# Optimization experiments

Hardware: AMD Instinct MI355X
Metric: run time of the kernel (lower is better)

## Reference

```python
import jax, jax.numpy as jnp
import numpy as np

N = 100_000        # nodes
E = 1_600_000      # edges (avg degree 16)
D_IN = 128         # raw node feature dim
H = 64             # hidden dim
D_E = 8            # edge attr dim
C = 2              # classes for both heads (parity-game winner / strategy)


def setup_inputs() -> dict:
    key = jax.random.key(0)
    ks = jax.random.split(key, 16)
    rn = lambda k, shp, s: jax.random.normal(k, shp, jnp.float32) * s
    inv = lambda f: 1.0 / np.sqrt(f)
    return {
        "x": rn(ks[0], (N, D_IN), 1.0),
        "edge_index": jax.random.randint(ks[1], (2, E), 0, N),
        "edge_attr": rn(ks[2], (E, D_E), 1.0),
        # encode: Linear(D_IN -> H) + ReLU
        "W_enc": rn(ks[3], (D_IN, H), inv(D_IN)),
        "b_enc": jnp.zeros((H,), jnp.float32),
        # core: single-head GATConv
        "W_gat": rn(ks[4], (H, H), inv(H)),
        "a_src": rn(ks[5], (H,), inv(H)),
        "a_dst": rn(ks[6], (H,), inv(H)),
        # node_classifier: MLP H -> H -> C
        "Wn1": rn(ks[7], (H, H), inv(H)),
        "bn1": jnp.zeros((H,), jnp.float32),
        "Wn2": rn(ks[8], (H, C), inv(H)),
        "bn2": jnp.zeros((C,), jnp.float32),
        # edge_classifier: MLP (2H + D_E) -> H -> C
        "We1": rn(ks[9], (2 * H + D_E, H), inv(2 * H + D_E)),
        "be1": jnp.zeros((H,), jnp.float32),
        "We2": rn(ks[10], (H, C), inv(H)),
        "be2": jnp.zeros((C,), jnp.float32),
    }


def _gat_core(h, src, dst, W_gat, a_src, a_dst):
    # Single-head GAT layer with segment softmax over incoming edges per dst.
    hg = h @ W_gat                                    # [N, H]
    hs, hd = hg[src], hg[dst]                         # [E, H] gathers
    scores = jax.nn.leaky_relu(hs @ a_src + hd @ a_dst, 0.2)  # [E]
    m = jax.ops.segment_max(scores, dst, num_segments=N)      # [N]
    m = jnp.where(jnp.isneginf(m), 0.0, m)            # guard isolated nodes
    ex = jnp.exp(scores - m[dst])                     # [E]
    denom = jax.ops.segment_sum(ex, dst, num_segments=N)      # [N]
    alpha = ex / (denom[dst] + 1e-9)                  # [E]
    agg = jax.ops.segment_sum(alpha[:, None] * hs, dst, num_segments=N)  # [N, H]
    return jax.nn.relu(agg)


def reference(x, edge_index, edge_attr, W_enc, b_enc, W_gat, a_src, a_dst,
              Wn1, bn1, Wn2, bn2, We1, be1, We2, be2):
    src, dst = edge_index[0], edge_index[1]
    # encode
    h = jax.nn.relu(x @ W_enc + b_enc)                # [N, H]
    # core (GATConv)
    xc = _gat_core(h, src, dst, W_gat, a_src, a_dst)  # [N, H]
    # node head
    node_logits = jax.nn.relu(xc @ Wn1 + bn1) @ Wn2 + bn2        # [N, C]
    # gather src/dst + concat edge_attr, edge head
    edge_feat = jnp.concatenate([xc[src], xc[dst], edge_attr], axis=-1)  # [E, 2H+D_E]
    edge_logits = jax.nn.relu(edge_feat @ We1 + be1) @ We2 + be2  # [E, C]
    return node_logits, edge_logits
```

## Files before the change

### kernel.cpp

```cpp
#include <hip/hip_runtime.h>
#include <hip/hip_bf16.h>

#define NN   100000
#define EE   1600000
#define DIN  128
#define HH   64
#define DEA  8
#define NCLS 2
#define BSZ  128
#define NBUCK ((NN + BSZ - 1) / BSZ)
#define CAPG 2368
#define CAP  4096
#define NCHUNK 100
#define CHUNK (EE / NCHUNK)

typedef __hip_bfloat16 bf16;
typedef short  short8 __attribute__((ext_vector_type(8)));
typedef float  f32x4  __attribute__((ext_vector_type(4)));

__device__ __forceinline__ void bf2x(unsigned u, float& lo, float& hi) {
    union { unsigned i; float f; } a, b;
    a.i = u << 16; b.i = u & 0xffff0000u;
    lo = a.f; hi = b.f;
}
__device__ __forceinline__ short f2bs(float f) {
    unsigned u = __float_as_uint(f);
    return (short)((u + 0x7fffu + ((u >> 16) & 1u)) >> 16);
}
__device__ __forceinline__ short8 cvt8(float4 a, float4 b) {
    short8 r;
    r[0] = f2bs(a.x); r[1] = f2bs(a.y); r[2] = f2bs(a.z); r[3] = f2bs(a.w);
    r[4] = f2bs(b.x); r[5] = f2bs(b.y); r[6] = f2bs(b.z); r[7] = f2bs(b.w);
    return r;
}
__device__ __forceinline__ f32x4 z4() {
    f32x4 z; z[0] = 0.f; z[1] = 0.f; z[2] = 0.f; z[3] = 0.f; return z;
}

#define WE_STRIDE 136
#define WG_STRIDE 72
#define TB_STRIDE 68
__global__ __launch_bounds__(256) void k_encode(
        const float* __restrict__ x,
        const float* __restrict__ W_enc, const float* __restrict__ b_enc,
        const float* __restrict__ W_gat,
        const float* __restrict__ a_src, const float* __restrict__ a_dst,
        bf16* __restrict__ hg_, float* __restrict__ s_src, float* __restrict__ s_dst) {
    __shared__ short wencT[64 * WE_STRIDE];
    __shared__ short wgatT[64 * WG_STRIDE];
    __shared__ float tb[4][16 * TB_STRIDE];
    short* hg = (short*)hg_;
    int tid = threadIdx.x;
    for (int i = tid; i < DIN * HH; i += 256) {
        int k = i >> 6, n = i & 63;
        wencT[n * WE_STRIDE + k] = f2bs(W_enc[i]);
    }
    for (int i = tid; i < HH * HH; i += 256) {
        int k = i >> 6, n = i & 63;
        wgatT[n * WG_STRIDE + k] = f2bs(W_gat[i]);
    }
    __syncthreads();
    int w = tid >> 6, l = tid & 63, m = l & 15, h = l >> 4;
    short8 wg[2][4];
    #pragma unroll
    for (int kt = 0; kt < 2; kt++)
        #pragma unroll
        for (int nt = 0; nt < 4; nt++)
            wg[kt][nt] = *(short8*)&wgatT[(nt * 16 + m) * WG_STRIDE + kt * 32 + h * 8];
    float avs[4], avd[4], ben[4];
    #pragma unroll
    for (int nt = 0; nt < 4; nt++) {
        avs[nt] = a_src[nt * 16 + m];
        avd[nt] = a_dst[nt * 16 + m];
        ben[nt] = b_enc[nt * 16 + m];
    }
    int tp = blockIdx.x * 4 + w;
    if (tp >= NN / 32) return;
    int n0 = tp * 32;
    float* tbw = tb[w];

    f32x4 acc1[2][4];
    #pragma unroll
    for (int rt = 0; rt < 2; rt++)
        #pragma unroll
        for (int nt = 0; nt < 4; nt++) acc1[rt][nt] = z4();
    #pragma unroll
    for (int kt = 0; kt < 4; kt++) {
        short8 af[2];
        #pragma unroll
        for (int rt = 0; rt < 2; rt++) {
            const float* xp = &x[(size_t)(n0 + rt * 16 + m) * DIN + kt * 32 + h * 8];
            af[rt] = cvt8(*(const float4*)xp, *(const float4*)(xp + 4));
        }
        #pragma unroll
        for (int nt = 0; nt < 4; nt++) {
            short8 bf = *(short8*)&wencT[(nt * 16 + m) * WE_STRIDE + kt * 32 + h * 8];
            acc1[0][nt] = __builtin_amdgcn_mfma_f32_16x16x32_bf16(af[0], bf, acc1[0][nt], 0, 0, 0);
            acc1[1][nt] = __builtin_amdgcn_mfma_f32_16x16x32_bf16(af[1], bf, acc1[1][nt], 0, 0, 0);
        }
    }
    #pragma unroll
    for (int rt = 0; rt < 2; rt++) {
        #pragma unroll
        for (int nt = 0; nt < 4; nt++)
            #pragma unroll
            for (int r = 0; r < 4; r++) {
                float hv = fmaxf(acc1[rt][nt][r] + ben[nt], 0.f);
                tbw[(h * 4 + r) * TB_STRIDE + nt * 16 + m] = hv;
            }
        f32x4 acc2[4];
        #pragma unroll
        for (int nt = 0; nt < 4; nt++) acc2[nt] = z4();
        #pragma unroll
        for (int kt = 0; kt < 2; kt++) {
            const float* tp_ = &tbw[m * TB_STRIDE + kt * 32 + h * 8];
            short8 af2 = cvt8(*(const float4*)tp_, *(const float4*)(tp_ + 4));
            #pragma unroll
            for (int nt = 0; nt < 4; nt++)
                acc2[nt] = __builtin_amdgcn_mfma_f32_16x16x32_bf16(af2, wg[kt][nt], acc2[nt], 0, 0, 0);
        }
        float ps[4] = {0.f, 0.f, 0.f, 0.f}, pd[4] = {0.f, 0.f, 0.f, 0.f};
        #pragma unroll
        for (int nt = 0; nt < 4; nt++)
            #pragma unroll
            for (int r = 0; r < 4; r++) {
                float v = acc2[nt][r];
                ps[r] = fmaf(v, avs[nt], ps[r]);
                pd[r] = fmaf(v, avd[nt], pd[r]);
                hg[(size_t)(n0 + rt * 16 + h * 4 + r) * HH + nt * 16 + m] = f2bs(v);
            }
        #pragma unroll
        for (int off = 1; off < 16; off <<= 1)
            #pragma unroll
            for (int r = 0; r < 4; r++) {
                ps[r] += __shfl_xor(ps[r], off);
                pd[r] += __shfl_xor(pd[r], off);
            }
        if (m == 0) {
            *(float4*)&s_src[n0 + rt * 16 + h * 4] = make_float4(ps[0], ps[1], ps[2], ps[3]);
            *(float4*)&s_dst[n0 + rt * 16 + h * 4] = make_float4(pd[0], pd[1], pd[2], pd[3]);
        }
    }
}

__global__ __launch_bounds__(256) void k_cvt(const float* __restrict__ attr,
                                             short* __restrict__ attr16) {
    int i = blockIdx.x * blockDim.x + threadIdx.x;
    int stride = gridDim.x * blockDim.x;
    for (int j = i; j < EE * DEA / 8; j += stride) {
        const float4* p = (const float4*)(attr + (size_t)j * 8);
        *(short8*)(attr16 + (size_t)j * 8) = cvt8(p[0], p[1]);
    }
}

__global__ __launch_bounds__(1024) void k_cscatter(
        const int* __restrict__ src, const int* __restrict__ dst,
        int* bcur, unsigned* __restrict__ ebuf) {
    __shared__ int cnt[NBUCK];
    __shared__ int cur[NBUCK];
    int tid = threadIdx.x;
    int e0 = blockIdx.x * CHUNK;
    for (int i = tid; i < NBUCK; i += 1024) cnt[i] = 0;
    __syncthreads();
    for (int i = tid; i < CHUNK; i += 1024)
        atomicAdd(&cnt[dst[e0 + i] >> 7], 1);
    __syncthreads();
    for (int i = tid; i < NBUCK; i += 1024) {
        int c = cnt[i];
        int base = c ? atomicAdd(&bcur[i], c) : 0;
        cur[i] = i * CAPG + base;
    }
    __syncthreads();
    for (int i = tid; i < CHUNK; i += 1024) {
        int dv = dst[e0 + i], sv = src[e0 + i];
        int b  = dv >> 7;
        int dl = dv & (BSZ - 1);
        int pos = atomicAdd(&cur[b], 1);
        ebuf[pos] = ((unsigned)dl << 24) | (unsigned)sv;
    }
}

__global__ __launch_bounds__(512) void k_bagg2(
        const unsigned* __restrict__ ebuf, const int* __restrict__ bcur,
        const float* __restrict__ s_src, const float* __restrict__ s_dst,
        const bf16* __restrict__ hg, bf16* __restrict__ agg_) {
    __shared__ unsigned sl[CAP];
    __shared__ int cnt[BSZ];
    __shared__ int sstart[BSZ];
    __shared__ int spos[BSZ];
    __shared__ int sscan[BSZ];
    short* agg = (short*)agg_;
    int tid = threadIdx.x;
    int b = blockIdx.x;
    int rs = b * CAPG;
    int ne = min(bcur[b], CAP);
    for (int i = tid; i < BSZ; i += 512) cnt[i] = 0;
    __syncthreads();
    for (int i = tid; i < ne; i += 512)
        atomicAdd(&cnt[ebuf[rs + i] >> 24], 1);
    __syncthreads();
    int v = (tid < BSZ) ? cnt[tid] : 0;
    if (tid < BSZ) sscan[tid] = v;
    __syncthreads();
    for (int s = 1; s < BSZ; s <<= 1) {
        int add = (tid < BSZ && tid >= s) ? sscan[tid - s] : 0;
        __syncthreads();
        if (tid < BSZ) sscan[tid] += add;
        __syncthreads();
    }
    if (tid < BSZ) { sstart[tid] = sscan[tid] - v; spos[tid] = sscan[tid] - v; }
    __syncthreads();
    for (int i = tid; i < ne; i += 512) {
        unsigned p = ebuf[rs + i];
        int dl = p >> 24;
        int q = atomicAdd(&spos[dl], 1);
        sl[q] = p & 0xFFFFFFu;
    }
    __syncthreads();
    int lane = tid & 63, wv = tid >> 6;
    int lane8 = lane & 7, grp = lane >> 3;
    for (int dl = wv; dl < BSZ; dl += 8) {
        int node = b * BSZ + dl;
        if (node >= NN) break;
        int st = sstart[dl], deg = cnt[dl];
        float sd = s_dst[node];
        float a[8] = {0.f}, denom = 0.f;
        for (int i = grp; i < deg; i += 8) {
            int sv = sl[st + i];
            float s = s_src[sv] + sd;
            s = (s >= 0.f) ? s : 0.2f * s;
            float ex = __expf(s);
            denom += ex;
            uint4 u = *(const uint4*)&hg[(size_t)sv * HH + lane8 * 8];
            float f0, f1, f2, f3, f4, f5, f6, f7;
            bf2x(u.x, f0, f1); bf2x(u.y, f2, f3);
            bf2x(u.z, f4, f5); bf2x(u.w, f6, f7);
            a[0] = fmaf(ex, f0, a[0]); a[1] = fmaf(ex, f1, a[1]);
            a[2] = fmaf(ex, f2, a[2]); a[3] = fmaf(ex, f3, a[3]);
            a[4] = fmaf(ex, f4, a[4]); a[5] = fmaf(ex, f5, a[5]);
            a[6] = fmaf(ex, f6, a[6]); a[7] = fmaf(ex, f7, a[7]);
        }
        #pragma unroll
        for (int off = 8; off < 64; off <<= 1) {
            #pragma unroll
            for (int j = 0; j < 8; j++) a[j] += __shfl_xor(a[j], off);
            denom += __shfl_xor(denom, off);
        }
        if (lane < 8) {
            float inv = 1.f / (denom + 1e-9f);
            short8 r;
            #pragma unroll
            for (int j = 0; j < 8; j++) r[j] = f2bs(a[j] * inv);
            *(short8*)&agg[(size_t)node * HH + lane8 * 8] = r;
        }
    }
}

#define WC_STRIDE 72
__global__ __launch_bounds__(256) void k_nodehead(
        const bf16* __restrict__ agg_,
        const float* __restrict__ Wn1, const float* __restrict__ bn1,
        const float* __restrict__ Wn2, const float* __restrict__ bn2,
        const float* __restrict__ We1,
        bf16* __restrict__ p_src_, bf16* __restrict__ p_dst_, float* __restrict__ out_node) {
    __shared__ short wcatT[192 * WC_STRIDE];
    const short* agg = (const short*)agg_;
    short* p_src = (short*)p_src_;
    short* p_dst = (short*)p_dst_;
    int tid = threadIdx.x;
    for (int i = tid; i < 3 * HH * HH; i += 256) {
        int mat = i >> 12, j = i & 4095;
        int k = j >> 6, l2 = j & 63;
        float v = (mat == 0) ? Wn1[j] : (mat == 1 ? We1[j] : We1[HH * HH + j]);
        wcatT[(mat * 64 + l2) * WC_STRIDE + k] = f2bs(v);
    }
    __syncthreads();
    int w = tid >> 6, l = tid & 63, m = l & 15, h = l >> 4;
    int tp = blockIdx.x * 4 + w;
    if (tp >= NN / 32) return;
    int n0 = tp * 32;
    float ben[4], wn2a[4], wn2b[4];
    #pragma unroll
    for (int nt = 0; nt < 4; nt++) {
        ben[nt]  = bn1[nt * 16 + m];
        wn2a[nt] = Wn2[(nt * 16 + m) * NCLS + 0];
        wn2b[nt] = Wn2[(nt * 16 + m) * NCLS + 1];
    }
    float bn20 = bn2[0], bn21 = bn2[1];
    #pragma unroll
    for (int rt = 0; rt < 2; rt++) {
        f32x4 acc[12];
        #pragma unroll
        for (int nt = 0; nt < 12; nt++) acc[nt] = z4();
        #pragma unroll
        for (int kt = 0; kt < 2; kt++) {
            short8 v = *(const short8*)&agg[(size_t)(n0 + rt * 16 + m) * HH + kt * 32 + h * 8];
            short8 af;
            #pragma unroll
            for (int j = 0; j < 8; j++) af[j] = (v[j] < 0) ? (short)0 : v[j];
            #pragma unroll
            for (int nt = 0; nt < 12; nt++) {
                short8 bf = *(short8*)&wcatT[(nt * 16 + m) * WC_STRIDE + kt * 32 + h * 8];
                acc[nt] = __builtin_amdgcn_mfma_f32_16x16x32_bf16(af, bf, acc[nt], 0, 0, 0);
            }
        }
        float l0[4] = {0.f, 0.f, 0.f, 0.f}, l1[4] = {0.f, 0.f, 0.f, 0.f};
        #pragma unroll
        for (int nt = 0; nt < 4; nt++)
            #pragma unroll
            for (int r = 0; r < 4; r++) {
                float t = fmaxf(acc[nt][r] + ben[nt], 0.f);
                l0[r] = fmaf(t, wn2a[nt], l0[r]);
                l1[r] = fmaf(t, wn2b[nt], l1[r]);
            }
        #pragma unroll
        for (int nt = 0; nt < 4; nt++)
            #pragma unroll
            for (int r = 0; r < 4; r++) {
                size_t row = (size_t)(n0 + rt * 16 + h * 4 + r) * HH + nt * 16 + m;
                p_src[row] = f2bs(acc[nt + 4][r]);
                p_dst[row] = f2bs(acc[nt + 8][r]);
            }
        #pragma unroll
        for (int off = 1; off < 16; off <<= 1)
            #pragma unroll
            for (int r = 0; r < 4; r++) {
                l0[r] += __shfl_xor(l0[r], off);
                l1[r] += __shfl_xor(l1[r], off);
            }
        if (m == 0) {
            #pragma unroll
            for (int r = 0; r < 4; r++)
                *(float2*)&out_node[(size_t)(n0 + rt * 16 + h * 4 + r) * NCLS] =
                    make_float2(l0[r] + bn20, l1[r] + bn21);
        }
    }
}

template<bool A16>
__global__ __launch_bounds__(256) void k_edgehead(
        const int* __restrict__ src, const int* __restrict__ dst,
        const float* __restrict__ edge_attr, const short* __restrict__ attr16,
        const bf16* __restrict__ p_src, const bf16* __restrict__ p_dst,
        const float* __restrict__ We1, const float* __restrict__ be1,
        const float* __restrict__ We2, const float* __restrict__ be2,
        float* __restrict__ out_edge) {
    int tid = threadIdx.x;
    int lane16 = tid & 15;
    int grp    = (tid & 63) >> 4;
    int wave   = tid >> 6;
    float w1a[DEA][4], w2c0[4], w2c1[4], b1v[4];
    #pragma unroll
    for (int d = 0; d < DEA; d++) {
        float4 v = *(const float4*)&We1[(2 * HH + d) * HH + lane16 * 4];
        w1a[d][0] = v.x; w1a[d][1] = v.y; w1a[d][2] = v.z; w1a[d][3] = v.w;
    }
    float4 bv = *(const float4*)&be1[lane16 * 4];
    b1v[0] = bv.x; b1v[1] = bv.y; b1v[2] = bv.z; b1v[3] = bv.w;
    #pragma unroll
    for (int j = 0; j < 4; j++) {
        w2c0[j] = We2[(lane16 * 4 + j) * NCLS + 0];
        w2c1[j] = We2[(lane16 * 4 + j) * NCLS + 1];
    }
    float be20 = be2[0], be21 = be2[1];

    int stride = gridDim.x * 64;
    for (int e = blockIdx.x * 64 + wave * 16 + grp * 4; e < EE; e += stride) {
        int sv[4], dv[4];
        #pragma unroll
        for (int q = 0; q < 4; q++) { sv[q] = src[e + q]; dv[q] = dst[e + q]; }
        uint2 us[4], ud[4];
        uint4 ua[4];
        float4 at0[4], at1[4];
        #pragma unroll
        for (int q = 0; q < 4; q++) {
            us[q] = *(const uint2*)&p_src[(size_t)sv[q] * HH + lane16 * 4];
            ud[q] = *(const uint2*)&p_dst[(size_t)dv[q] * HH + lane16 * 4];
            if constexpr (A16) {
                ua[q] = *(const uint4*)&attr16[(size_t)(e + q) * DEA];
            } else {
                at0[q] = *(const float4*)&edge_attr[(size_t)(e + q) * DEA];
                at1[q] = *(const float4*)&edge_attr[(size_t)(e + q) * DEA + 4];
            }
        }
        float l0[4], l1[4];
        #pragma unroll
        for (int q = 0; q < 4; q++) {
            float s0, s1, s2, s3, d0, d1, d2, d3;
            bf2x(us[q].x, s0, s1); bf2x(us[q].y, s2, s3);
            bf2x(ud[q].x, d0, d1); bf2x(ud[q].y, d2, d3);
            float t[4] = {s0 + d0 + b1v[0], s1 + d1 + b1v[1],
                          s2 + d2 + b1v[2], s3 + d3 + b1v[3]};
            float av[DEA];
            if constexpr (A16) {
                bf2x(ua[q].x, av[0], av[1]); bf2x(ua[q].y, av[2], av[3]);
                bf2x(ua[q].z, av[4], av[5]); bf2x(ua[q].w, av[6], av[7]);
            } else {
                av[0] = at0[q].x; av[1] = at0[q].y; av[2] = at0[q].z; av[3] = at0[q].w;
                av[4] = at1[q].x; av[5] = at1[q].y; av[6] = at1[q].z; av[7] = at1[q].w;
            }
            l0[q] = 0.f; l1[q] = 0.f;
            #pragma unroll
            for (int j = 0; j < 4; j++) {
                #pragma unroll
                for (int d = 0; d < DEA; d++) t[j] = fmaf(av[d], w1a[d][j], t[j]);
                float r = fmaxf(t[j], 0.f);
                l0[q] = fmaf(r, w2c0[j], l0[q]);
                l1[q] = fmaf(r, w2c1[j], l1[q]);
            }
        }
        #pragma unroll
        for (int off = 8; off; off >>= 1)
            #pragma unroll
            for (int q = 0; q < 4; q++) {
                l0[q] += __shfl_xor(l0[q], off);
                l1[q] += __shfl_xor(l1[q], off);
            }
        if (lane16 == 0) {
            #pragma unroll
            for (int q = 0; q < 4; q++)
                *(float2*)&out_edge[(size_t)(e + q) * NCLS] =
                    make_float2(l0[q] + be20, l1[q] + be21);
        }
    }
}

extern "C" void kernel_launch(void* const* d_in, const int* in_sizes, int n_in,
                              void* d_out, int out_size, void* d_ws, size_t ws_size,
                              hipStream_t stream) {
    const float* x      = (const float*)d_in[0];
    const int*   ei     = (const int*)  d_in[1];
    const float* attr   = (const float*)d_in[2];
    const float* W_enc  = (const float*)d_in[3];
    const float* b_enc  = (const float*)d_in[4];
    const float* W_gat  = (const float*)d_in[5];
    const float* a_src  = (const float*)d_in[6];
    const float* a_dst  = (const float*)d_in[7];
    const float* Wn1    = (const float*)d_in[8];
    const float* bn1    = (const float*)d_in[9];
    const float* Wn2    = (const float*)d_in[10];
    const float* bn2    = (const float*)d_in[11];
    const float* We1    = (const float*)d_in[12];
    const float* be1    = (const float*)d_in[13];
    const float* We2    = (const float*)d_in[14];
    const float* be2    = (const float*)d_in[15];
    float* out = (float*)d_out;
    float* ws  = (float*)d_ws;

    bf16*     hg_psrc = (bf16*)ws;
    bf16*     agg     = (bf16*)(ws + (size_t)NN * 32);
    bf16*     p_dst   = (bf16*)(ws + (size_t)NN * 64);
    float*    ssrc    = ws + (size_t)NN * 96;
    float*    sdst    = ssrc + NN;
    int*      bcur    = (int*)(sdst + NN);
    unsigned* ebuf    = (unsigned*)(bcur + 1024);
    short*    attr16  = (short*)(ebuf + (size_t)NBUCK * CAPG);
    size_t    need    = (size_t)((char*)(attr16 + (size_t)EE * DEA) - (char*)ws);
    bool      a16     = ws_size >= need;

    const int* srcp = ei;
    const int* dstp = ei + EE;

    hipMemsetAsync(bcur, 0, NBUCK * sizeof(int), stream);
    k_encode  <<<782, 256, 0, stream>>>(x, W_enc, b_enc, W_gat, a_src, a_dst,
                                        hg_psrc, ssrc, sdst);
    if (a16)
        k_cvt <<<2048, 256, 0, stream>>>(attr, attr16);
    k_cscatter<<<NCHUNK, 1024, 0, stream>>>(srcp, dstp, bcur, ebuf);
    k_bagg2   <<<NBUCK, 512, 0, stream>>>(ebuf, bcur, ssrc, sdst, hg_psrc, agg);
    k_nodehead<<<782, 256, 0, stream>>>(agg, Wn1, bn1, Wn2, bn2, We1,
                                        hg_psrc , p_dst, out);
    if (a16)
        k_edgehead<true><<<8192, 256, 0, stream>>>(srcp, dstp, attr, attr16,
                                                   hg_psrc, p_dst, We1, be1, We2, be2,
                                                   out + (size_t)NN * NCLS);
    else
        k_edgehead<false><<<8192, 256, 0, stream>>>(srcp, dstp, attr, nullptr,
                                                    hg_psrc, p_dst, We1, be1, We2, be2,
                                                    out + (size_t)NN * NCLS);
}
```

Before: 211.3 us.

## Merge encode, edge scatter and attr conversion into one block-specialized front kernel

```diff
diff --git a/kernel.cpp b/kernel.cpp
--- a/kernel.cpp
+++ b/kernel.cpp
@@ -10,9 +10,10 @@
 #define BSZ  128
 #define NBUCK ((NN + BSZ - 1) / BSZ)
 #define CAPG 2368
-#define CAP  4096
 #define NCHUNK 100
 #define CHUNK (EE / NCHUNK)
+#define NENC 391
+#define NCVT 160
 
 typedef __hip_bfloat16 bf16;
 typedef short  short8 __attribute__((ext_vector_type(8)));
@@ -40,143 +41,152 @@
 #define WE_STRIDE 136
 #define WG_STRIDE 72
 #define TB_STRIDE 68
-__global__ __launch_bounds__(256) void k_encode(
+union FrontLDS {
+    struct {
+        short wencT[64 * WE_STRIDE];
+        short wgatT[64 * WG_STRIDE];
+        float tb[8][16 * TB_STRIDE];
+    } e;
+    struct {
+        int cnt[NBUCK];
+        int cur[NBUCK];
+    } s;
+};
+
+__global__ __launch_bounds__(512) void k_front(
         const float* __restrict__ x,
         const float* __restrict__ W_enc, const float* __restrict__ b_enc,
         const float* __restrict__ W_gat,
         const float* __restrict__ a_src, const float* __restrict__ a_dst,
-        bf16* __restrict__ hg_, float* __restrict__ s_src, float* __restrict__ s_dst) {
-    __shared__ short wencT[64 * WE_STRIDE];
-    __shared__ short wgatT[64 * WG_STRIDE];
-    __shared__ float tb[4][16 * TB_STRIDE];
-    short* hg = (short*)hg_;
+        bf16* __restrict__ hg_, float* __restrict__ s_src, float* __restrict__ s_dst,
+        const int* __restrict__ src, const int* __restrict__ dst,
+        int* bcur, unsigned* __restrict__ ebuf,
+        const float* __restrict__ attr, short* __restrict__ attr16) {
+    __shared__ FrontLDS u;
+    int bid = blockIdx.x;
     int tid = threadIdx.x;
-    for (int i = tid; i < DIN * HH; i += 256) {
-        int k = i >> 6, n = i & 63;
-        wencT[n * WE_STRIDE + k] = f2bs(W_enc[i]);
-    }
-    for (int i = tid; i < HH * HH; i += 256) {
-        int k = i >> 6, n = i & 63;
-        wgatT[n * WG_STRIDE + k] = f2bs(W_gat[i]);
-    }
-    __syncthreads();
-    int w = tid >> 6, l = tid & 63, m = l & 15, h = l >> 4;
-    short8 wg[2][4];
-    #pragma unroll
-    for (int kt = 0; kt < 2; kt++)
-        #pragma unroll
-        for (int nt = 0; nt < 4; nt++)
-            wg[kt][nt] = *(short8*)&wgatT[(nt * 16 + m) * WG_STRIDE + kt * 32 + h * 8];
-    float avs[4], avd[4], ben[4];
-    #pragma unroll
-    for (int nt = 0; nt < 4; nt++) {
-        avs[nt] = a_src[nt * 16 + m];
-        avd[nt] = a_dst[nt * 16 + m];
-        ben[nt] = b_enc[nt * 16 + m];
-    }
-    int tp = blockIdx.x * 4 + w;
-    if (tp >= NN / 32) return;
-    int n0 = tp * 32;
-    float* tbw = tb[w];
-
-    f32x4 acc1[2][4];
-    #pragma unroll
-    for (int rt = 0; rt < 2; rt++)
-        #pragma unroll
-        for (int nt = 0; nt < 4; nt++) acc1[rt][nt] = z4();
-    #pragma unroll
-    for (int kt = 0; kt < 4; kt++) {
-        short8 af[2];
+
+    if (bid < NENC) {
+        short* hg = (short*)hg_;
+        for (int i = tid; i < DIN * HH; i += 512) {
+            int k = i >> 6, n = i & 63;
+            u.e.wencT[n * WE_STRIDE + k] = f2bs(W_enc[i]);
+        }
+        for (int i = tid; i < HH * HH; i += 512) {
+            int k = i >> 6, n = i & 63;
+            u.e.wgatT[n * WG_STRIDE + k] = f2bs(W_gat[i]);
+        }
+        __syncthreads();
+        int w = tid >> 6, l = tid & 63, m = l & 15, h = l >> 4;
+        short8 wg[2][4];
+        #pragma unroll
+        for (int kt = 0; kt < 2; kt++)
+            #pragma unroll
+            for (int nt = 0; nt < 4; nt++)
+                wg[kt][nt] = *(short8*)&u.e.wgatT[(nt * 16 + m) * WG_STRIDE + kt * 32 + h * 8];
+        float avs[4], avd[4], ben[4];
+        #pragma unroll
+        for (int nt = 0; nt < 4; nt++) {
+            avs[nt] = a_src[nt * 16 + m];
+            avd[nt] = a_dst[nt * 16 + m];
+            ben[nt] = b_enc[nt * 16 + m];
+        }
+        int tp = bid * 8 + w;
+        if (tp >= NN / 32) return;
+        int n0 = tp * 32;
+        float* tbw = u.e.tb[w];
+
+        f32x4 acc1[2][4];
+        #pragma unroll
+        for (int rt = 0; rt < 2; rt++)
+            #pragma unroll
+            for (int nt = 0; nt < 4; nt++) acc1[rt][nt] = z4();
+        #pragma unroll
+        for (int kt = 0; kt < 4; kt++) {
+            short8 af[2];
+            #pragma unroll
+            for (int rt = 0; rt < 2; rt++) {
+                const float* xp = &x[(size_t)(n0 + rt * 16 + m) * DIN + kt * 32 + h * 8];
+                af[rt] = cvt8(*(const float4*)xp, *(const float4*)(xp + 4));
+            }
+            #pragma unroll
+            for (int nt = 0; nt < 4; nt++) {
+                short8 bf = *(short8*)&u.e.wencT[(nt * 16 + m) * WE_STRIDE + kt * 32 + h * 8];
+                acc1[0][nt] = __builtin_amdgcn_mfma_f32_16x16x32_bf16(af[0], bf, acc1[0][nt], 0, 0, 0);
+                acc1[1][nt] = __builtin_amdgcn_mfma_f32_16x16x32_bf16(af[1], bf, acc1[1][nt], 0, 0, 0);
+            }
+        }
         #pragma unroll
         for (int rt = 0; rt < 2; rt++) {
-            const float* xp = &x[(size_t)(n0 + rt * 16 + m) * DIN + kt * 32 + h * 8];
-            af[rt] = cvt8(*(const float4*)xp, *(const float4*)(xp + 4));
-        }
-        #pragma unroll
-        for (int nt = 0; nt < 4; nt++) {
-            short8 bf = *(short8*)&wencT[(nt * 16 + m) * WE_STRIDE + kt * 32 + h * 8];
-            acc1[0][nt] = __builtin_amdgcn_mfma_f32_16x16x32_bf16(af[0], bf, acc1[0][nt], 0, 0, 0);
-            acc1[1][nt] = __builtin_amdgcn_mfma_f32_16x16x32_bf16(af[1], bf, acc1[1][nt], 0, 0, 0);
-        }
-    }
-    #pragma unroll
-    for (int rt = 0; rt < 2; rt++) {
-        #pragma unroll
-        for (int nt = 0; nt < 4; nt++)
-            #pragma unroll
-            for (int r = 0; r < 4; r++) {
-                float hv = fmaxf(acc1[rt][nt][r] + ben[nt], 0.f);
-                tbw[(h * 4 + r) * TB_STRIDE + nt * 16 + m] = hv;
-            }
-        f32x4 acc2[4];
-        #pragma unroll
-        for (int nt = 0; nt < 4; nt++) acc2[nt] = z4();
-        #pragma unroll
-        for (int kt = 0; kt < 2; kt++) {
-            const float* tp_ = &tbw[m * TB_STRIDE + kt * 32 + h * 8];
-            short8 af2 = cvt8(*(const float4*)tp_, *(const float4*)(tp_ + 4));
             #pragma unroll
             for (int nt = 0; nt < 4; nt++)
-                acc2[nt] = __builtin_amdgcn_mfma_f32_16x16x32_bf16(af2, wg[kt][nt], acc2[nt], 0, 0, 0);
-        }
-        float ps[4] = {0.f, 0.f, 0.f, 0.f}, pd[4] = {0.f, 0.f, 0.f, 0.f};
-        #pragma unroll
-        for (int nt = 0; nt < 4; nt++)
-            #pragma unroll
-            for (int r = 0; r < 4; r++) {
-                float v = acc2[nt][r];
-                ps[r] = fmaf(v, avs[nt], ps[r]);
-                pd[r] = fmaf(v, avd[nt], pd[r]);
-                hg[(size_t)(n0 + rt * 16 + h * 4 + r) * HH + nt * 16 + m] = f2bs(v);
-            }
-        #pragma unroll
-        for (int off = 1; off < 16; off <<= 1)
-            #pragma unroll
-            for (int r = 0; r < 4; r++) {
-                ps[r] += __shfl_xor(ps[r], off);
-                pd[r] += __shfl_xor(pd[r], off);
-            }
-        if (m == 0) {
-            *(float4*)&s_src[n0 + rt * 16 + h * 4] = make_float4(ps[0], ps[1], ps[2], ps[3]);
-            *(float4*)&s_dst[n0 + rt * 16 + h * 4] = make_float4(pd[0], pd[1], pd[2], pd[3]);
-        }
-    }
-}
-
-__global__ __launch_bounds__(256) void k_cvt(const float* __restrict__ attr,
-                                             short* __restrict__ attr16) {
-    int i = blockIdx.x * blockDim.x + threadIdx.x;
-    int stride = gridDim.x * blockDim.x;
-    for (int j = i; j < EE * DEA / 8; j += stride) {
-        const float4* p = (const float4*)(attr + (size_t)j * 8);
-        *(short8*)(attr16 + (size_t)j * 8) = cvt8(p[0], p[1]);
-    }
-}
-
-__global__ __launch_bounds__(1024) void k_cscatter(
-        const int* __restrict__ src, const int* __restrict__ dst,
-        int* bcur, unsigned* __restrict__ ebuf) {
-    __shared__ int cnt[NBUCK];
-    __shared__ int cur[NBUCK];
-    int tid = threadIdx.x;
-    int e0 = blockIdx.x * CHUNK;
-    for (int i = tid; i < NBUCK; i += 1024) cnt[i] = 0;
-    __syncthreads();
-    for (int i = tid; i < CHUNK; i += 1024)
-        atomicAdd(&cnt[dst[e0 + i] >> 7], 1);
-    __syncthreads();
-    for (int i = tid; i < NBUCK; i += 1024) {
-        int c = cnt[i];
-        int base = c ? atomicAdd(&bcur[i], c) : 0;
-        cur[i] = i * CAPG + base;
-    }
-    __syncthreads();
-    for (int i = tid; i < CHUNK; i += 1024) {
-        int dv = dst[e0 + i], sv = src[e0 + i];
-        int b  = dv >> 7;
-        int dl = dv & (BSZ - 1);
-        int pos = atomicAdd(&cur[b], 1);
-        ebuf[pos] = ((unsigned)dl << 24) | (unsigned)sv;
+                #pragma unroll
+                for (int r = 0; r < 4; r++) {
+                    float hv = fmaxf(acc1[rt][nt][r] + ben[nt], 0.f);
+                    tbw[(h * 4 + r) * TB_STRIDE + nt * 16 + m] = hv;
+                }
+            f32x4 acc2[4];
+            #pragma unroll
+            for (int nt = 0; nt < 4; nt++) acc2[nt] = z4();
+            #pragma unroll
+            for (int kt = 0; kt < 2; kt++) {
+                const float* pptr = &tbw[m * TB_STRIDE + kt * 32 + h * 8];
+                short8 af2 = cvt8(*(const float4*)pptr, *(const float4*)(pptr + 4));
+                #pragma unroll
+                for (int nt = 0; nt < 4; nt++)
+                    acc2[nt] = __builtin_amdgcn_mfma_f32_16x16x32_bf16(af2, wg[kt][nt], acc2[nt], 0, 0, 0);
+            }
+            float ps[4] = {0.f, 0.f, 0.f, 0.f}, pd[4] = {0.f, 0.f, 0.f, 0.f};
+            #pragma unroll
+            for (int nt = 0; nt < 4; nt++)
+                #pragma unroll
+                for (int r = 0; r < 4; r++) {
+                    float v = acc2[nt][r];
+                    ps[r] = fmaf(v, avs[nt], ps[r]);
+                    pd[r] = fmaf(v, avd[nt], pd[r]);
+                    hg[(size_t)(n0 + rt * 16 + h * 4 + r) * HH + nt * 16 + m] = f2bs(v);
+                }
+            #pragma unroll
+            for (int off = 1; off < 16; off <<= 1)
+                #pragma unroll
+                for (int r = 0; r < 4; r++) {
+                    ps[r] += __shfl_xor(ps[r], off);
+                    pd[r] += __shfl_xor(pd[r], off);
+                }
+            if (m == 0) {
+                *(float4*)&s_src[n0 + rt * 16 + h * 4] = make_float4(ps[0], ps[1], ps[2], ps[3]);
+                *(float4*)&s_dst[n0 + rt * 16 + h * 4] = make_float4(pd[0], pd[1], pd[2], pd[3]);
+            }
+        }
+    } else if (bid < NENC + NCHUNK) {
+        int cb = bid - NENC;
+        int e0 = cb * CHUNK;
+        for (int i = tid; i < NBUCK; i += 512) u.s.cnt[i] = 0;
+        __syncthreads();
+        for (int i = tid; i < CHUNK; i += 512)
+            atomicAdd(&u.s.cnt[dst[e0 + i] >> 7], 1);
+        __syncthreads();
+        for (int i = tid; i < NBUCK; i += 512) {
+            int c = u.s.cnt[i];
+            int base = c ? atomicAdd(&bcur[i], c) : 0;
+            u.s.cur[i] = i * CAPG + base;
+        }
+        __syncthreads();
+        for (int i = tid; i < CHUNK; i += 512) {
+            int dv = dst[e0 + i], sv = src[e0 + i];
+            int b  = dv >> 7;
+            int dl = dv & (BSZ - 1);
+            int pos = atomicAdd(&u.s.cur[b], 1);
+            ebuf[pos] = ((unsigned)dl << 24) | (unsigned)sv;
+        }
+    } else {
+        if (!attr16) return;
+        int cvb = bid - NENC - NCHUNK;
+        int stride = NCVT * 512;
+        for (int j = cvb * 512 + tid; j < EE * DEA / 8; j += stride) {
+            const float4* p = (const float4*)(attr + (size_t)j * 8);
+            *(short8*)(attr16 + (size_t)j * 8) = cvt8(p[0], p[1]);
+        }
     }
 }
 
@@ -184,7 +194,7 @@
         const unsigned* __restrict__ ebuf, const int* __restrict__ bcur,
         const float* __restrict__ s_src, const float* __restrict__ s_dst,
         const bf16* __restrict__ hg, bf16* __restrict__ agg_) {
-    __shared__ unsigned sl[CAP];
+    __shared__ unsigned sl[CAPG];
     __shared__ int cnt[BSZ];
     __shared__ int sstart[BSZ];
     __shared__ int spos[BSZ];
@@ -193,7 +203,7 @@
     int tid = threadIdx.x;
     int b = blockIdx.x;
     int rs = b * CAPG;
-    int ne = min(bcur[b], CAP);
+    int ne = min(bcur[b], CAPG);
     for (int i = tid; i < BSZ; i += 512) cnt[i] = 0;
     __syncthreads();
     for (int i = tid; i < ne; i += 512)
@@ -231,10 +241,10 @@
             s = (s >= 0.f) ? s : 0.2f * s;
             float ex = __expf(s);
             denom += ex;
-            uint4 u = *(const uint4*)&hg[(size_t)sv * HH + lane8 * 8];
+            uint4 uu = *(const uint4*)&hg[(size_t)sv * HH + lane8 * 8];
             float f0, f1, f2, f3, f4, f5, f6, f7;
-            bf2x(u.x, f0, f1); bf2x(u.y, f2, f3);
-            bf2x(u.z, f4, f5); bf2x(u.w, f6, f7);
+            bf2x(uu.x, f0, f1); bf2x(uu.y, f2, f3);
+            bf2x(uu.z, f4, f5); bf2x(uu.w, f6, f7);
             a[0] = fmaf(ex, f0, a[0]); a[1] = fmaf(ex, f1, a[1]);
             a[2] = fmaf(ex, f2, a[2]); a[3] = fmaf(ex, f3, a[3]);
             a[4] = fmaf(ex, f4, a[4]); a[5] = fmaf(ex, f5, a[5]);
@@ -462,11 +472,11 @@
     const int* dstp = ei + EE;
 
     hipMemsetAsync(bcur, 0, NBUCK * sizeof(int), stream);
-    k_encode  <<<782, 256, 0, stream>>>(x, W_enc, b_enc, W_gat, a_src, a_dst,
-                                        hg_psrc, ssrc, sdst);
-    if (a16)
-        k_cvt <<<2048, 256, 0, stream>>>(attr, attr16);
-    k_cscatter<<<NCHUNK, 1024, 0, stream>>>(srcp, dstp, bcur, ebuf);
+    int front_blocks = NENC + NCHUNK + (a16 ? NCVT : 0);
+    k_front   <<<front_blocks, 512, 0, stream>>>(x, W_enc, b_enc, W_gat, a_src, a_dst,
+                                                 hg_psrc, ssrc, sdst,
+                                                 srcp, dstp, bcur, ebuf,
+                                                 attr, a16 ? attr16 : nullptr);
     k_bagg2   <<<NBUCK, 512, 0, stream>>>(ebuf, bcur, ssrc, sdst, hg_psrc, agg);
     k_nodehead<<<782, 256, 0, stream>>>(agg, Wn1, bn1, Wn2, bn2, We1,
                                         hg_psrc , p_dst, out);
```

Result: faster. 194.0 us, median of 2 (-8.2%).

## Split bucket scatter into histogram, scan and deterministic scatter; add nontemporal loads

Applied to the files above, without the earlier changes.

```diff
diff --git a/kernel.cpp b/kernel.cpp
--- a/kernel.cpp
+++ b/kernel.cpp
@@ -10,13 +10,15 @@
 #define BSZ  128
 #define NBUCK ((NN + BSZ - 1) / BSZ)
 #define CAPG 2368
-#define CAP  4096
-#define NCHUNK 100
+#define NCHUNK 250
 #define CHUNK (EE / NCHUNK)
 
 typedef __hip_bfloat16 bf16;
-typedef short  short8 __attribute__((ext_vector_type(8)));
-typedef float  f32x4  __attribute__((ext_vector_type(4)));
+typedef short    short8 __attribute__((ext_vector_type(8)));
+typedef float    f32x4  __attribute__((ext_vector_type(4)));
+typedef float    f32x4e __attribute__((ext_vector_type(4)));
+typedef float    f32x2e __attribute__((ext_vector_type(2)));
+typedef unsigned u32x4e __attribute__((ext_vector_type(4)));
 
 __device__ __forceinline__ void bf2x(unsigned u, float& lo, float& hi) {
     union { unsigned i; float f; } a, b;
@@ -31,6 +33,12 @@
     short8 r;
     r[0] = f2bs(a.x); r[1] = f2bs(a.y); r[2] = f2bs(a.z); r[3] = f2bs(a.w);
     r[4] = f2bs(b.x); r[5] = f2bs(b.y); r[6] = f2bs(b.z); r[7] = f2bs(b.w);
+    return r;
+}
+__device__ __forceinline__ short8 cvt8e(f32x4e a, f32x4e b) {
+    short8 r;
+    r[0] = f2bs(a[0]); r[1] = f2bs(a[1]); r[2] = f2bs(a[2]); r[3] = f2bs(a[3]);
+    r[4] = f2bs(b[0]); r[5] = f2bs(b[1]); r[6] = f2bs(b[2]); r[7] = f2bs(b[3]);
     return r;
 }
 __device__ __forceinline__ f32x4 z4() {
@@ -148,28 +156,56 @@
     int i = blockIdx.x * blockDim.x + threadIdx.x;
     int stride = gridDim.x * blockDim.x;
     for (int j = i; j < EE * DEA / 8; j += stride) {
-        const float4* p = (const float4*)(attr + (size_t)j * 8);
-        *(short8*)(attr16 + (size_t)j * 8) = cvt8(p[0], p[1]);
-    }
-}
-
-__global__ __launch_bounds__(1024) void k_cscatter(
+        const f32x4e* p = (const f32x4e*)(attr + (size_t)j * 8);
+        f32x4e a = __builtin_nontemporal_load(p);
+        f32x4e b = __builtin_nontemporal_load(p + 1);
+        __builtin_nontemporal_store(cvt8e(a, b), (short8*)(attr16 + (size_t)j * 8));
+    }
+}
+
+__global__ __launch_bounds__(1024) void k_hist(const int* __restrict__ dst,
+                                               int* __restrict__ gcnt) {
+    __shared__ int h[NBUCK];
+    int tid = threadIdx.x;
+    int c = blockIdx.x;
+    int e0 = c * CHUNK;
+    for (int i = tid; i < NBUCK; i += 1024) h[i] = 0;
+    __syncthreads();
+    for (int i = tid; i < CHUNK; i += 1024)
+        atomicAdd(&h[dst[e0 + i] >> 7], 1);
+    __syncthreads();
+    for (int i = tid; i < NBUCK; i += 1024)
+        gcnt[c * NBUCK + i] = h[i];
+}
+
+__global__ __launch_bounds__(256) void k_scan(const int* __restrict__ gcnt,
+                                              int* __restrict__ gbase,
+                                              int* __restrict__ btot) {
+    __shared__ int sm[256];
+    int b = blockIdx.x;
+    int c = threadIdx.x;
+    int v = (c < NCHUNK) ? gcnt[c * NBUCK + b] : 0;
+    sm[c] = v;
+    __syncthreads();
+    for (int s = 1; s < 256; s <<= 1) {
+        int add = (c >= s) ? sm[c - s] : 0;
+        __syncthreads();
+        sm[c] += add;
+        __syncthreads();
+    }
+    if (c < NCHUNK) gbase[c * NBUCK + b] = sm[c] - v;
+    if (c == 255) btot[b] = sm[255];
+}
+
+__global__ __launch_bounds__(1024) void k_scatter3(
         const int* __restrict__ src, const int* __restrict__ dst,
-        int* bcur, unsigned* __restrict__ ebuf) {
-    __shared__ int cnt[NBUCK];
+        const int* __restrict__ gbase, unsigned* __restrict__ ebuf) {
     __shared__ int cur[NBUCK];
     int tid = threadIdx.x;
-    int e0 = blockIdx.x * CHUNK;
-    for (int i = tid; i < NBUCK; i += 1024) cnt[i] = 0;
-    __syncthreads();
-    for (int i = tid; i < CHUNK; i += 1024)
-        atomicAdd(&cnt[dst[e0 + i] >> 7], 1);
-    __syncthreads();
-    for (int i = tid; i < NBUCK; i += 1024) {
-        int c = cnt[i];
-        int base = c ? atomicAdd(&bcur[i], c) : 0;
-        cur[i] = i * CAPG + base;
-    }
+    int c = blockIdx.x;
+    int e0 = c * CHUNK;
+    for (int i = tid; i < NBUCK; i += 1024)
+        cur[i] = i * CAPG + gbase[c * NBUCK + i];
     __syncthreads();
     for (int i = tid; i < CHUNK; i += 1024) {
         int dv = dst[e0 + i], sv = src[e0 + i];
@@ -181,10 +217,10 @@
 }
 
 __global__ __launch_bounds__(512) void k_bagg2(
-        const unsigned* __restrict__ ebuf, const int* __restrict__ bcur,
+        const unsigned* __restrict__ ebuf, const int* __restrict__ btot,
         const float* __restrict__ s_src, const float* __restrict__ s_dst,
         const bf16* __restrict__ hg, bf16* __restrict__ agg_) {
-    __shared__ unsigned sl[CAP];
+    __shared__ unsigned sl[CAPG];
     __shared__ int cnt[BSZ];
     __shared__ int sstart[BSZ];
     __shared__ int spos[BSZ];
@@ -193,7 +229,7 @@
     int tid = threadIdx.x;
     int b = blockIdx.x;
     int rs = b * CAPG;
-    int ne = min(bcur[b], CAP);
+    int ne = min(btot[b], CAPG);
     for (int i = tid; i < BSZ; i += 512) cnt[i] = 0;
     __syncthreads();
     for (int i = tid; i < ne; i += 512)
@@ -231,10 +267,10 @@
             s = (s >= 0.f) ? s : 0.2f * s;
             float ex = __expf(s);
             denom += ex;
-            uint4 u = *(const uint4*)&hg[(size_t)sv * HH + lane8 * 8];
+            uint4 uu = *(const uint4*)&hg[(size_t)sv * HH + lane8 * 8];
             float f0, f1, f2, f3, f4, f5, f6, f7;
-            bf2x(u.x, f0, f1); bf2x(u.y, f2, f3);
-            bf2x(u.z, f4, f5); bf2x(u.w, f6, f7);
+            bf2x(uu.x, f0, f1); bf2x(uu.y, f2, f3);
+            bf2x(uu.z, f4, f5); bf2x(uu.w, f6, f7);
             a[0] = fmaf(ex, f0, a[0]); a[1] = fmaf(ex, f1, a[1]);
             a[2] = fmaf(ex, f2, a[2]); a[3] = fmaf(ex, f3, a[3]);
             a[4] = fmaf(ex, f4, a[4]); a[5] = fmaf(ex, f5, a[5]);
@@ -368,16 +404,20 @@
     for (int e = blockIdx.x * 64 + wave * 16 + grp * 4; e < EE; e += stride) {
         int sv[4], dv[4];
         #pragma unroll
-        for (int q = 0; q < 4; q++) { sv[q] = src[e + q]; dv[q] = dst[e + q]; }
+        for (int q = 0; q < 4; q++) {
+            sv[q] = __builtin_nontemporal_load(&src[e + q]);
+            dv[q] = __builtin_nontemporal_load(&dst[e + q]);
+        }
         uint2 us[4], ud[4];
-        uint4 ua[4];
+        u32x4e ua[4];
         float4 at0[4], at1[4];
         #pragma unroll
         for (int q = 0; q < 4; q++) {
             us[q] = *(const uint2*)&p_src[(size_t)sv[q] * HH + lane16 * 4];
             ud[q] = *(const uint2*)&p_dst[(size_t)dv[q] * HH + lane16 * 4];
             if constexpr (A16) {
-                ua[q] = *(const uint4*)&attr16[(size_t)(e + q) * DEA];
+                ua[q] = __builtin_nontemporal_load(
+                            (const u32x4e*)&attr16[(size_t)(e + q) * DEA]);
             } else {
                 at0[q] = *(const float4*)&edge_attr[(size_t)(e + q) * DEA];
                 at1[q] = *(const float4*)&edge_attr[(size_t)(e + q) * DEA + 4];
@@ -393,8 +433,8 @@
                           s2 + d2 + b1v[2], s3 + d3 + b1v[3]};
             float av[DEA];
             if constexpr (A16) {
-                bf2x(ua[q].x, av[0], av[1]); bf2x(ua[q].y, av[2], av[3]);
-                bf2x(ua[q].z, av[4], av[5]); bf2x(ua[q].w, av[6], av[7]);
+                bf2x(ua[q][0], av[0], av[1]); bf2x(ua[q][1], av[2], av[3]);
+                bf2x(ua[q][2], av[4], av[5]); bf2x(ua[q][3], av[6], av[7]);
             } else {
                 av[0] = at0[q].x; av[1] = at0[q].y; av[2] = at0[q].z; av[3] = at0[q].w;
                 av[4] = at1[q].x; av[5] = at1[q].y; av[6] = at1[q].z; av[7] = at1[q].w;
@@ -418,9 +458,10 @@
             }
         if (lane16 == 0) {
             #pragma unroll
-            for (int q = 0; q < 4; q++)
-                *(float2*)&out_edge[(size_t)(e + q) * NCLS] =
-                    make_float2(l0[q] + be20, l1[q] + be21);
+            for (int q = 0; q < 4; q++) {
+                f32x2e r; r[0] = l0[q] + be20; r[1] = l1[q] + be21;
+                __builtin_nontemporal_store(r, (f32x2e*)&out_edge[(size_t)(e + q) * NCLS]);
+            }
         }
     }
 }
@@ -452,8 +493,10 @@
     bf16*     p_dst   = (bf16*)(ws + (size_t)NN * 64);
     float*    ssrc    = ws + (size_t)NN * 96;
     float*    sdst    = ssrc + NN;
-    int*      bcur    = (int*)(sdst + NN);
-    unsigned* ebuf    = (unsigned*)(bcur + 1024);
+    int*      gcnt    = (int*)(sdst + NN);
+    int*      gbase   = gcnt + NCHUNK * NBUCK;
+    int*      btot    = gbase + NCHUNK * NBUCK;
+    unsigned* ebuf    = (unsigned*)(btot + 1024);
     short*    attr16  = (short*)(ebuf + (size_t)NBUCK * CAPG);
     size_t    need    = (size_t)((char*)(attr16 + (size_t)EE * DEA) - (char*)ws);
     bool      a16     = ws_size >= need;
@@ -461,13 +504,14 @@
     const int* srcp = ei;
     const int* dstp = ei + EE;
 
-    hipMemsetAsync(bcur, 0, NBUCK * sizeof(int), stream);
     k_encode  <<<782, 256, 0, stream>>>(x, W_enc, b_enc, W_gat, a_src, a_dst,
                                         hg_psrc, ssrc, sdst);
+    k_hist    <<<NCHUNK, 1024, 0, stream>>>(dstp, gcnt);
+    k_scan    <<<NBUCK, 256, 0, stream>>>(gcnt, gbase, btot);
+    k_scatter3<<<NCHUNK, 1024, 0, stream>>>(srcp, dstp, gbase, ebuf);
     if (a16)
         k_cvt <<<2048, 256, 0, stream>>>(attr, attr16);
-    k_cscatter<<<NCHUNK, 1024, 0, stream>>>(srcp, dstp, bcur, ebuf);
-    k_bagg2   <<<NBUCK, 512, 0, stream>>>(ebuf, bcur, ssrc, sdst, hg_psrc, agg);
+    k_bagg2   <<<NBUCK, 512, 0, stream>>>(ebuf, btot, ssrc, sdst, hg_psrc, agg);
     k_nodehead<<<782, 256, 0, stream>>>(agg, Wn1, bn1, Wn2, bn2, We1,
                                         hg_psrc , p_dst, out);
     if (a16)
```

Result: slower. 223.6 us (+5.8%).
